# Performance work log

Measured on AMD Instinct MI355X. Metric: run time of the kernel, lower is better.

Reference implementation:

```python
import jax, jax.numpy as jnp
import numpy as np

L, N, T = 2048, 32, 200
V, IN, H, Q = 34, 512, 256, 256


def setup_inputs() -> dict:
    key = jax.random.key(0)
    ks = jax.random.split(key, 16)
    s = 0.05
    def rn(i, shape):
        return jax.random.normal(ks[i], shape, dtype=jnp.float32) * s
    zeros = lambda shape: jnp.zeros(shape, jnp.float32)
    return {
        "seqs": jax.random.normal(ks[0], (L, N, IN), dtype=jnp.float32),
        "seq_lens": L // 2 + jax.random.randint(ks[1], (N,), 0, L // 2),
        "label_in": jax.random.randint(ks[2], (N, T), 0, V),
        "embedding": rn(3, (V, H)),
        "inith": zeros((3, H)),
        "initc": zeros((3, H)),
        "W_ih0": rn(4, (4 * H, 2 * H)), "W_hh0": rn(5, (4 * H, H)),
        "b_ih0": zeros((4 * H,)), "b_hh0": zeros((4 * H,)),
        "W_ih1": rn(6, (4 * H, H)), "W_hh1": rn(7, (4 * H, H)),
        "b_ih1": zeros((4 * H,)), "b_hh1": zeros((4 * H,)),
        "W_ih2": rn(8, (4 * H, H)), "W_hh2": rn(9, (4 * H, H)),
        "b_ih2": zeros((4 * H,)), "b_hh2": zeros((4 * H,)),
        "Wq": rn(10, (Q, H)), "bq": zeros((Q,)),
        "Wk": rn(11, (Q, IN)), "bk": zeros((Q,)),
        "Wv": rn(12, (H, IN)), "bv": zeros((H,)),
        "Wo1": rn(13, (H, H + Q)), "bo1": zeros((H,)),
        "bo2": zeros((V,)),
    }


def _lstm_cell(x, h, c, Wih, Whh, bih, bhh):
    # torch.nn.LSTMCell gate math (i, f, g, o ordering)
    g = x @ Wih.T + bih + h @ Whh.T + bhh
    i, f, gg, o = jnp.split(g, 4, axis=-1)
    c_new = jax.nn.sigmoid(f) * c + jax.nn.sigmoid(i) * jnp.tanh(gg)
    h_new = jax.nn.sigmoid(o) * jnp.tanh(c_new)
    return h_new, c_new


def reference(seqs, seq_lens, label_in, embedding, inith, initc,
              W_ih0, W_hh0, b_ih0, b_hh0, W_ih1, W_hh1, b_ih1, b_hh1,
              W_ih2, W_hh2, b_ih2, b_hh2, Wq, bq, Wk, bk, Wv, bv, Wo1, bo1, bo2):
    Lk, Nk = seqs.shape[0], seqs.shape[1]
    Hh = inith.shape[1]

    # key/value projections: (L,N,IN) -> (N,L,Q) / (N,L,H)
    key_t = jnp.einsum('lni,qi->nlq', seqs, Wk) + bk
    val_t = jnp.einsum('lni,hi->nlh', seqs, Wv) + bv
    mask = (jnp.arange(Lk)[None, :] < seq_lens[:, None]).astype(seqs.dtype)  # (N,L)

    def attend(q):
        scores = jnp.einsum('nlq,nq->nl', key_t, q)
        attn = jax.nn.softmax(scores, axis=1)
        # faithful to torch: mask AFTER softmax, clamp, renormalize
        attn = jnp.maximum(attn * mask, 1e-9)
        attn = attn / attn.sum(axis=1, keepdims=True)
        return jnp.einsum('nl,nlh->nh', attn, val_t)

    h0 = jnp.broadcast_to(inith[0], (Nk, Hh)); c0 = jnp.broadcast_to(initc[0], (Nk, Hh))
    h1 = jnp.broadcast_to(inith[1], (Nk, Hh)); c1 = jnp.broadcast_to(initc[1], (Nk, Hh))
    h2 = jnp.broadcast_to(inith[2], (Nk, Hh)); c2 = jnp.broadcast_to(initc[2], (Nk, Hh))

    ctx = attend(h2 @ Wq.T + bq)
    emb = jnp.swapaxes(embedding[label_in], 0, 1)  # (T,N,H)

    def step(carry, x):
        h0, c0, h1, c1, h2, c2, ctx = carry
        rnn_in = jnp.concatenate([ctx, x], axis=1)  # (N, 2H)
        h0, c0 = _lstm_cell(rnn_in, h0, c0, W_ih0, W_hh0, b_ih0, b_hh0)
        h1, c1 = _lstm_cell(h0, h1, c1, W_ih1, W_hh1, b_ih1, b_hh1)
        h2, c2 = _lstm_cell(h1, h2, c2, W_ih2, W_hh2, b_ih2, b_hh2)
        q = h2 @ Wq.T + bq
        ctx = attend(q)
        hid = jnp.concatenate([ctx, q], axis=1) @ Wo1.T + bo1
        logit = hid @ embedding.T + bo2  # tied output weight
        return (h0, c0, h1, c1, h2, c2, ctx), logit

    _, logits = jax.lax.scan(step, (h0, c0, h1, c1, h2, c2, ctx), emb)
    return logits  # (T, N, V)
```

## Files before the change

kernel.cpp:

```cpp
#include <hip/hip_runtime.h>
#include <stdint.h>


typedef __attribute__((ext_vector_type(8))) short short8;
typedef __attribute__((ext_vector_type(4))) short short4v;
typedef __attribute__((ext_vector_type(4))) float float4v;

__device__ __forceinline__ float b2f(unsigned short u) {
  union { unsigned u; float f; } x; x.u = ((unsigned)u) << 16; return x.f;
}
__device__ __forceinline__ unsigned short f2b(float f) {
  union { float f; unsigned u; } x; x.f = f;
  unsigned r = (x.u + 0x7fffu + ((x.u >> 16) & 1u)) >> 16;
  return (unsigned short)r;
}
__device__ __forceinline__ float sigm(float x) { return 1.f / (1.f + __expf(-x)); }
__device__ __forceinline__ float tanh_s(float x) { return 1.f - 2.f / (__expf(2.f * x) + 1.f); }

static constexpr size_t OFF_K2   = 0;
static constexpr size_t OFF_VAL  = OFF_K2  + 33554432;
static constexpr size_t OFF_WK2  = OFF_VAL + 33554432;
static constexpr size_t OFF_BK2  = OFF_WK2 + 262144;
static constexpr size_t OFF_WKB  = OFF_BK2 + 1024;
static constexpr size_t OFF_BQBK = OFF_WKB + 2048;
static constexpr size_t OFF_KB   = OFF_BQBK + 256;
static constexpr size_t OFF_CTXA = OFF_KB  + 262144;
static constexpr size_t OFF_CTXS = OFF_CTXA + 6586368;
static constexpr size_t OFF_H2A  = OFF_CTXS + 25856;
static constexpr size_t OFF_HST  = OFF_H2A + 3276800;
static constexpr size_t OFF_CST  = OFF_HST + 98304;
static constexpr size_t OFF_FLAG = OFF_CST + 98304;
static constexpr size_t OFF_C    = OFF_FLAG + 256;
static constexpr size_t cEMB   = OFF_C;
static constexpr size_t cINITH = cEMB   + 17408;
static constexpr size_t cINITC = cINITH + 1536;
static constexpr size_t cWIH0  = cINITC + 1536;
static constexpr size_t cWHH0  = cWIH0  + 1048576;
static constexpr size_t cBIH0  = cWHH0  + 524288;
static constexpr size_t cBHH0  = cBIH0  + 2048;
static constexpr size_t cWIH1  = cBHH0  + 2048;
static constexpr size_t cWHH1  = cWIH1  + 524288;
static constexpr size_t cBIH1  = cWHH1  + 524288;
static constexpr size_t cBHH1  = cBIH1  + 2048;
static constexpr size_t cWIH2  = cBHH1  + 2048;
static constexpr size_t cWHH2  = cWIH2  + 524288;
static constexpr size_t cBIH2  = cWHH2  + 524288;
static constexpr size_t cBHH2  = cBIH2  + 2048;
static constexpr size_t cWQ    = cBHH2  + 2048;
static constexpr size_t cBQ    = cWQ    + 131072;
static constexpr size_t cWK    = cBQ    + 512;
static constexpr size_t cBK    = cWK    + 262144;
static constexpr size_t cWV    = cBK    + 512;
static constexpr size_t cBV    = cWV    + 262144;
static constexpr size_t cWO1   = cBV    + 512;
static constexpr size_t cBO1   = cWO1   + 262144;
static constexpr size_t cBO2   = cBO1   + 512;
static constexpr size_t WS_REQ = cBO2 + 128;

__global__ void k_sentinel(unsigned short* out, int n) {
  int i = blockIdx.x * 256 + threadIdx.x;
  if (i < n) out[i] = f2b(12345.0f);
}

__global__ void k_detect(const unsigned* __restrict__ seqw, int* flag) {
  int lane = threadIdx.x;
  unsigned w = seqw[lane];
  float lo = b2f((unsigned short)(w & 0xFFFFu));
  float a = fabsf(lo);
  bool ok = (a > 1e-3f) && (a < 4.0f);
  unsigned long long m = __ballot(ok);
  if (lane == 0) *flag = (__popcll((unsigned long long)m) >= 32) ? 1 : 0;
}

struct ConvList {
  const void* src[24];
  unsigned long long dstoff[24];
  int n[24];
};
__global__ void k_conv(ConvList cl, char* ws, const int* __restrict__ flag) {
  const int ti = blockIdx.y;
  const int i = blockIdx.x * 256 + threadIdx.x;
  const int n = cl.n[ti];
  if (i >= n) return;
  unsigned short* dst = (unsigned short*)(ws + cl.dstoff[ti]);
  if (*flag) dst[i] = ((const unsigned short*)cl.src[ti])[i];
  else       dst[i] = f2b(((const float*)cl.src[ti])[i]);
}

__global__ void k_p0(const unsigned short* __restrict__ Wq, const unsigned short* __restrict__ Wk,
                     const unsigned short* __restrict__ bq, const unsigned short* __restrict__ bk,
                     unsigned short* Wk2, float* bk2, float* wkb, float* bqbk) {
  int wg = blockIdx.x, tid = threadIdx.x;
  if (wg < 512) {
    int idx = wg * 256 + tid;
    int h = idx >> 9, j = idx & 511;
    float acc = 0.f;
    for (int i = 0; i < 256; ++i) acc += b2f(Wq[i * 256 + h]) * b2f(Wk[i * 512 + j]);
    Wk2[h * 512 + j] = f2b(acc);
  } else if (wg == 512) {
    float acc = 0.f;
    for (int i = 0; i < 256; ++i) acc += b2f(bk[i]) * b2f(Wq[i * 256 + tid]);
    bk2[tid] = acc;
  } else if (wg == 513) {
    for (int j = tid; j < 512; j += 256) {
      float acc = 0.f;
      for (int i = 0; i < 256; ++i) acc += b2f(bq[i]) * b2f(Wk[i * 512 + j]);
      wkb[j] = acc;
    }
  } else {
    if (tid == 0) {
      float acc = 0.f;
      for (int i = 0; i < 256; ++i) acc += b2f(bq[i]) * b2f(bk[i]);
      *bqbk = acc;
    }
  }
}

__global__ void k_init(const void* __restrict__ seqsv, const int* __restrict__ flag,
                       const unsigned short* __restrict__ inith, const unsigned short* __restrict__ initc,
                       const float* __restrict__ wkb, const float* __restrict__ bqbk, float* KB,
                       float* ctxacc, float* ctxsum, unsigned short* hst, float* cst) {
  int gid = blockIdx.x * 256 + threadIdx.x;
  for (int i = gid; i < 201 * 8192; i += 131072) ctxacc[i] = 0.f;
  if (gid < 6432) ctxsum[gid] = 0.f;
  if (gid < 8192) {
    int j = gid & 255;
    for (int Lr = 0; Lr < 3; ++Lr) {
      unsigned short hv = inith[Lr * 256 + j];
      hst[Lr * 16384 + gid] = hv;
      hst[Lr * 16384 + 8192 + gid] = hv;
      cst[Lr * 8192 + gid] = b2f(initc[Lr * 256 + j]);
    }
  }
  if (gid < 65536) {
    int l = gid >> 5, n = gid & 31;
    float acc = *bqbk;
    if (*flag) {
      const short8* row = (const short8*)((const unsigned short*)seqsv + (size_t)gid * 512);
      for (int jj = 0; jj < 64; ++jj) {
        short8 s = row[jj];
        #pragma unroll
        for (int e = 0; e < 8; ++e) acc += b2f((unsigned short)s[e]) * wkb[jj * 8 + e];
      }
    } else {
      const float4v* row = (const float4v*)((const float*)seqsv + (size_t)gid * 512);
      for (int jj = 0; jj < 128; ++jj) {
        float4v s = row[jj];
        acc += s.x * wkb[jj * 4 + 0] + s.y * wkb[jj * 4 + 1]
             + s.z * wkb[jj * 4 + 2] + s.w * wkb[jj * 4 + 3];
      }
    }
    KB[n * 2048 + l] = acc;
  }
}

__global__ __launch_bounds__(256) void k_gemm(
    const void* __restrict__ Aseqv, const int* __restrict__ flag,
    const unsigned short* __restrict__ Wk2,
    const unsigned short* __restrict__ Wv, const float* __restrict__ bk2,
    const unsigned short* __restrict__ bv, unsigned short* __restrict__ K2,
    unsigned short* __restrict__ VALo) {
  __shared__ short As[5120];
  __shared__ short Bs[5120];
  const int tid = threadIdx.x;
  const int lane = tid & 63, wid = tid >> 6;
  const int c0 = blockIdx.x * 128;
  const int m0 = blockIdx.y * 128;
  const unsigned short* Wb = (c0 < 256) ? Wk2 : Wv;
  const int cb = c0 & 255;
  const int srow = tid >> 1, skh = (tid & 1) * 16;
  const int m = lane & 15, q = lane >> 4;
  const bool isf32 = (*flag == 0);

  float4v zero = {0.f, 0.f, 0.f, 0.f};
  float4v acc[2][8];
  for (int i = 0; i < 2; ++i) for (int j = 0; j < 8; ++j) acc[i][j] = zero;

  for (int it = 0; it < 16; ++it) {
    const int k0 = it * 32;
    if (isf32) {
      const float4v* sa = (const float4v*)((const float*)Aseqv + (size_t)(m0 + srow) * 512 + k0 + skh);
      float4v u0 = sa[0], u1 = sa[1], u2 = sa[2], u3 = sa[3];
      short8 s0, s1;
      s0[0]=(short)f2b(u0.x); s0[1]=(short)f2b(u0.y); s0[2]=(short)f2b(u0.z); s0[3]=(short)f2b(u0.w);
      s0[4]=(short)f2b(u1.x); s0[5]=(short)f2b(u1.y); s0[6]=(short)f2b(u1.z); s0[7]=(short)f2b(u1.w);
      s1[0]=(short)f2b(u2.x); s1[1]=(short)f2b(u2.y); s1[2]=(short)f2b(u2.z); s1[3]=(short)f2b(u2.w);
      s1[4]=(short)f2b(u3.x); s1[5]=(short)f2b(u3.y); s1[6]=(short)f2b(u3.z); s1[7]=(short)f2b(u3.w);
      *(short8*)&As[srow * 40 + skh] = s0;
      *(short8*)&As[srow * 40 + skh + 8] = s1;
    } else {
      const short8* sa = (const short8*)((const unsigned short*)Aseqv + (size_t)(m0 + srow) * 512 + k0 + skh);
      *(short8*)&As[srow * 40 + skh] = sa[0];
      *(short8*)&As[srow * 40 + skh + 8] = sa[1];
    }
    const short8* sb = (const short8*)(Wb + (size_t)(cb + srow) * 512 + k0 + skh);
    *(short8*)&Bs[srow * 40 + skh] = sb[0];
    *(short8*)&Bs[srow * 40 + skh + 8] = sb[1];
    __syncthreads();
    short8 af[2], bf[8];
    #pragma unroll
    for (int i = 0; i < 2; ++i) af[i] = *(const short8*)&As[((wid * 2 + i) * 16 + m) * 40 + q * 8];
    #pragma unroll
    for (int j = 0; j < 8; ++j) bf[j] = *(const short8*)&Bs[(j * 16 + m) * 40 + q * 8];
    #pragma unroll
    for (int i = 0; i < 2; ++i)
      #pragma unroll
      for (int j = 0; j < 8; ++j)
        acc[i][j] = __builtin_amdgcn_mfma_f32_16x16x32_bf16(af[i], bf[j], acc[i][j], 0, 0, 0);
    __syncthreads();
  }
  const bool isK = (c0 < 256);
  #pragma unroll
  for (int i = 0; i < 2; ++i) {
    #pragma unroll
    for (int j = 0; j < 8; ++j) {
      const int colg = c0 + j * 16 + m;
      const float badd = isK ? bk2[colg] : b2f(bv[colg - 256]);
      #pragma unroll
      for (int r = 0; r < 4; ++r) {
        const int mm = m0 + (wid * 2 + i) * 16 + q * 4 + r;
        const int l = mm >> 5, n = mm & 31;
        const float v = acc[i][j][r] + badd;
        const size_t o = ((size_t)n * 2048 + l) * 256 + (isK ? colg : colg - 256);
        (isK ? K2 : VALo)[o] = f2b(v);
      }
    }
  }
}

__global__ __launch_bounds__(256) void k_attn(
    const int* __restrict__ seq_lens, const unsigned short* __restrict__ K2,
    const unsigned short* __restrict__ VAL, const float* __restrict__ KB,
    const unsigned short* __restrict__ h2src, float* __restrict__ ctxa_slot,
    float* __restrict__ ctxs_slot) {
  __shared__ float red[4][260];
  const int tid = threadIdx.x, wg = blockIdx.x;
  const int lane = tid & 63, wid = tid >> 6;
  const int n = wg >> 3, ch = wg & 7;
  const int len = seq_lens[n];
  const int l0 = ch << 8;
  int l1 = l0 + 256; if (l1 > len) l1 = len;
  const int hb = lane * 4;
  const float h0v = b2f(h2src[n * 256 + hb + 0]);
  const float h1v = b2f(h2src[n * 256 + hb + 1]);
  const float h2v = b2f(h2src[n * 256 + hb + 2]);
  const float h3v = b2f(h2src[n * 256 + hb + 3]);
  float a0 = 0.f, a1 = 0.f, a2 = 0.f, a3 = 0.f, se = 0.f;
  const float* kbn = KB + n * 2048;
  #pragma unroll 2
  for (int l = l0 + wid; l < l1; l += 4) {
    const size_t base = ((size_t)n * 2048 + l) * 256 + hb;
    const short4v kv = *(const short4v*)(K2 + base);
    float s = b2f((unsigned short)kv[0]) * h0v + b2f((unsigned short)kv[1]) * h1v
            + b2f((unsigned short)kv[2]) * h2v + b2f((unsigned short)kv[3]) * h3v;
    s += __shfl_xor(s, 1);  s += __shfl_xor(s, 2);  s += __shfl_xor(s, 4);
    s += __shfl_xor(s, 8);  s += __shfl_xor(s, 16); s += __shfl_xor(s, 32);
    float sc = s + kbn[l];
    sc = fminf(fmaxf(sc, -60.f), 60.f);
    const float e = __expf(sc);
    se += e;
    const short4v vv = *(const short4v*)(VAL + base);
    a0 += e * b2f((unsigned short)vv[0]); a1 += e * b2f((unsigned short)vv[1]);
    a2 += e * b2f((unsigned short)vv[2]); a3 += e * b2f((unsigned short)vv[3]);
  }
  red[wid][hb + 0] = a0; red[wid][hb + 1] = a1;
  red[wid][hb + 2] = a2; red[wid][hb + 3] = a3;
  if (lane == 0) red[wid][256] = se;
  __syncthreads();
  const float s = red[0][tid] + red[1][tid] + red[2][tid] + red[3][tid];
  atomicAdd(ctxa_slot + n * 256 + tid, s);
  if (tid == 0) {
    const float ssum = red[0][256] + red[1][256] + red[2][256] + red[3][256];
    atomicAdd(ctxs_slot + n, ssum);
  }
}

__global__ __launch_bounds__(256) void k_cell0(
    const float* __restrict__ ctxa_t, const float* __restrict__ ctxs_t,
    const int* __restrict__ label_in, int t, const unsigned short* __restrict__ emb,
    const unsigned short* __restrict__ Wih0, const unsigned short* __restrict__ Whh0,
    const unsigned short* __restrict__ bih0, const unsigned short* __restrict__ bhh0,
    const unsigned short* __restrict__ h0r, unsigned short* __restrict__ h0w,
    float* __restrict__ cst0) {
  __shared__ unsigned short lds_ctx[32 * 264];
  const int tid = threadIdx.x, wg = blockIdx.x;
  const int lane = tid & 63, wid = tid >> 6;
  for (int idx = tid; idx < 8192; idx += 256) {
    const int n = idx >> 8, k = idx & 255;
    lds_ctx[n * 264 + k] = f2b(ctxa_t[idx] / fmaxf(ctxs_t[n], 1e-30f));
  }
  __syncthreads();
  const int w = wg * 4 + wid;
  const int c = lane & 15, q = lane >> 4;
  const int grow = (c >> 2) * 256 + 4 * w + (c & 3);
  float4v ar0 = {0.f, 0.f, 0.f, 0.f}, ar1 = ar0;
  #pragma unroll
  for (int kk = 0; kk < 8; ++kk) {
    const int k = kk * 32 + q * 8;
    const short8 b = *(const short8*)(Wih0 + (size_t)grow * 512 + k);
    const short8 a0 = *(const short8*)&lds_ctx[c * 264 + k];
    const short8 a1 = *(const short8*)&lds_ctx[(c + 16) * 264 + k];
    ar0 = __builtin_amdgcn_mfma_f32_16x16x32_bf16(a0, b, ar0, 0, 0, 0);
    ar1 = __builtin_amdgcn_mfma_f32_16x16x32_bf16(a1, b, ar1, 0, 0, 0);
  }
  const int v0i = label_in[c * 200 + t];
  const int v1i = label_in[(c + 16) * 200 + t];
  const unsigned short* e0 = emb + (size_t)v0i * 256;
  const unsigned short* e1 = emb + (size_t)v1i * 256;
  #pragma unroll
  for (int kk = 0; kk < 8; ++kk) {
    const int k = kk * 32 + q * 8;
    const short8 b = *(const short8*)(Wih0 + (size_t)grow * 512 + 256 + k);
    const short8 a0 = *(const short8*)(e0 + k);
    const short8 a1 = *(const short8*)(e1 + k);
    ar0 = __builtin_amdgcn_mfma_f32_16x16x32_bf16(a0, b, ar0, 0, 0, 0);
    ar1 = __builtin_amdgcn_mfma_f32_16x16x32_bf16(a1, b, ar1, 0, 0, 0);
  }
  #pragma unroll
  for (int kk = 0; kk < 8; ++kk) {
    const int k = kk * 32 + q * 8;
    const short8 b = *(const short8*)(Whh0 + (size_t)grow * 256 + k);
    const short8 a0 = *(const short8*)(h0r + (size_t)c * 256 + k);
    const short8 a1 = *(const short8*)(h0r + (size_t)(c + 16) * 256 + k);
    ar0 = __builtin_amdgcn_mfma_f32_16x16x32_bf16(a0, b, ar0, 0, 0, 0);
    ar1 = __builtin_amdgcn_mfma_f32_16x16x32_bf16(a1, b, ar1, 0, 0, 0);
  }
  const float bias = b2f(bih0[grow]) + b2f(bhh0[grow]);
  const int d = c & 3, gt = c >> 2;
  #pragma unroll
  for (int mt = 0; mt < 2; ++mt) {
    const float4v av = mt ? ar1 : ar0;
    #pragma unroll
    for (int r = 0; r < 4; ++r) {
      const float g = av[r] + bias;
      const float gi = __shfl(g, (lane & 48) | d);
      const float gf = __shfl(g, (lane & 48) | (4 + d));
      const float gg = __shfl(g, (lane & 48) | (8 + d));
      const float go = __shfl(g, (lane & 48) | (12 + d));
      if (gt == 0) {
        const int n = mt * 16 + q * 4 + r;
        const int j = 4 * w + d;
        const float cold = cst0[n * 256 + j];
        const float cnew = sigm(gf) * cold + sigm(gi) * tanh_s(gg);
        const float hnew = sigm(go) * tanh_s(cnew);
        cst0[n * 256 + j] = cnew;
        h0w[n * 256 + j] = f2b(hnew);
      }
    }
  }
}

__global__ __launch_bounds__(256) void k_cell12(
    const unsigned short* __restrict__ Wih, const unsigned short* __restrict__ Whh,
    const unsigned short* __restrict__ bih, const unsigned short* __restrict__ bhh,
    const unsigned short* __restrict__ xsrc, const unsigned short* __restrict__ hsrc,
    float* __restrict__ cstate, unsigned short* __restrict__ hdst,
    unsigned short* __restrict__ h2dst) {
  const int tid = threadIdx.x, wg = blockIdx.x;
  const int lane = tid & 63, wid = tid >> 6;
  const int w = wg * 4 + wid;
  const int c = lane & 15, q = lane >> 4;
  const int grow = (c >> 2) * 256 + 4 * w + (c & 3);
  float4v ar0 = {0.f, 0.f, 0.f, 0.f}, ar1 = ar0;
  #pragma unroll
  for (int kk = 0; kk < 8; ++kk) {
    const int k = kk * 32 + q * 8;
    const short8 b = *(const short8*)(Wih + (size_t)grow * 256 + k);
    const short8 a0 = *(const short8*)(xsrc + (size_t)c * 256 + k);
    const short8 a1 = *(const short8*)(xsrc + (size_t)(c + 16) * 256 + k);
    ar0 = __builtin_amdgcn_mfma_f32_16x16x32_bf16(a0, b, ar0, 0, 0, 0);
    ar1 = __builtin_amdgcn_mfma_f32_16x16x32_bf16(a1, b, ar1, 0, 0, 0);
  }
  #pragma unroll
  for (int kk = 0; kk < 8; ++kk) {
    const int k = kk * 32 + q * 8;
    const short8 b = *(const short8*)(Whh + (size_t)grow * 256 + k);
    const short8 a0 = *(const short8*)(hsrc + (size_t)c * 256 + k);
    const short8 a1 = *(const short8*)(hsrc + (size_t)(c + 16) * 256 + k);
    ar0 = __builtin_amdgcn_mfma_f32_16x16x32_bf16(a0, b, ar0, 0, 0, 0);
    ar1 = __builtin_amdgcn_mfma_f32_16x16x32_bf16(a1, b, ar1, 0, 0, 0);
  }
  const float bias = b2f(bih[grow]) + b2f(bhh[grow]);
  const int d = c & 3, gt = c >> 2;
  #pragma unroll
  for (int mt = 0; mt < 2; ++mt) {
    const float4v av = mt ? ar1 : ar0;
    #pragma unroll
    for (int r = 0; r < 4; ++r) {
      const float g = av[r] + bias;
      const float gi = __shfl(g, (lane & 48) | d);
      const float gf = __shfl(g, (lane & 48) | (4 + d));
      const float gg = __shfl(g, (lane & 48) | (8 + d));
      const float go = __shfl(g, (lane & 48) | (12 + d));
      if (gt == 0) {
        const int n = mt * 16 + q * 4 + r;
        const int j = 4 * w + d;
        const float cold = cstate[n * 256 + j];
        const float cnew = sigm(gf) * cold + sigm(gi) * tanh_s(gg);
        const float hnew = sigm(go) * tanh_s(cnew);
        cstate[n * 256 + j] = cnew;
        hdst[n * 256 + j] = f2b(hnew);
        if (h2dst) h2dst[n * 256 + j] = f2b(hnew);
      }
    }
  }
}

__global__ __launch_bounds__(256) void k_out(
    const unsigned short* __restrict__ h2all, const float* __restrict__ ctxacc,
    const float* __restrict__ ctxsum,
    const unsigned short* __restrict__ Wq, const unsigned short* __restrict__ bq,
    const unsigned short* __restrict__ Wo1, const unsigned short* __restrict__ bo1,
    const unsigned short* __restrict__ emb, const unsigned short* __restrict__ bo2,
    void* __restrict__ outv, const int* __restrict__ flag) {
  const int wg = blockIdx.x, tid = threadIdx.x;
  const int g0 = wg * 4;
  __shared__ float z[4][512];
  __shared__ float hid[4][256];
  #pragma unroll
  for (int r = 0; r < 4; ++r) hid[r][tid] = b2f(h2all[(size_t)(g0 + r) * 256 + tid]);
  __syncthreads();
  {
    float qa[4] = {0.f, 0.f, 0.f, 0.f};
    const short8* wrow = (const short8*)(Wq + (size_t)tid * 256);
    for (int k8 = 0; k8 < 32; ++k8) {
      const short8 w = wrow[k8];
      float wf[8];
      #pragma unroll
      for (int e = 0; e < 8; ++e) wf[e] = b2f((unsigned short)w[e]);
      #pragma unroll
      for (int r = 0; r < 4; ++r) {
        const float* hz = &hid[r][k8 * 8];
        const float4v x0 = *(const float4v*)hz;
        const float4v x1 = *(const float4v*)(hz + 4);
        qa[r] += wf[0] * x0.x + wf[1] * x0.y + wf[2] * x0.z + wf[3] * x0.w
               + wf[4] * x1.x + wf[5] * x1.y + wf[6] * x1.z + wf[7] * x1.w;
      }
    }
    const float bqv = b2f(bq[tid]);
    #pragma unroll
    for (int r = 0; r < 4; ++r) z[r][256 + tid] = qa[r] + bqv;
    #pragma unroll
    for (int r = 0; r < 4; ++r) {
      const int row = g0 + r; const int tt = row >> 5; const int n = row & 31;
      const float ds = fmaxf(ctxsum[(tt + 1) * 32 + n], 1e-30f);
      z[r][tid] = ctxacc[(size_t)(tt + 1) * 8192 + n * 256 + tid] / ds;
    }
  }
  __syncthreads();
  {
    float ha[4] = {0.f, 0.f, 0.f, 0.f};
    const short8* wrow = (const short8*)(Wo1 + (size_t)tid * 512);
    for (int k8 = 0; k8 < 64; ++k8) {
      const short8 w = wrow[k8];
      float wf[8];
      #pragma unroll
      for (int e = 0; e < 8; ++e) wf[e] = b2f((unsigned short)w[e]);
      #pragma unroll
      for (int r = 0; r < 4; ++r) {
        const float* hz = &z[r][k8 * 8];
        const float4v x0 = *(const float4v*)hz;
        const float4v x1 = *(const float4v*)(hz + 4);
        ha[r] += wf[0] * x0.x + wf[1] * x0.y + wf[2] * x0.z + wf[3] * x0.w
               + wf[4] * x1.x + wf[5] * x1.y + wf[6] * x1.z + wf[7] * x1.w;
      }
    }
    const float bo = b2f(bo1[tid]);
    __syncthreads();
    #pragma unroll
    for (int r = 0; r < 4; ++r) hid[r][tid] = ha[r] + bo;
  }
  __syncthreads();
  if (tid < 136) {
    const int r = tid / 34, v = tid - r * 34;
    const unsigned short* er = emb + v * 256;
    float acc = b2f(bo2[v]);
    for (int h8 = 0; h8 < 32; ++h8) {
      const short8 ee = *(const short8*)(er + h8 * 8);
      const float* hz = &hid[r][h8 * 8];
      acc += b2f((unsigned short)ee[0]) * hz[0] + b2f((unsigned short)ee[1]) * hz[1]
           + b2f((unsigned short)ee[2]) * hz[2] + b2f((unsigned short)ee[3]) * hz[3]
           + b2f((unsigned short)ee[4]) * hz[4] + b2f((unsigned short)ee[5]) * hz[5]
           + b2f((unsigned short)ee[6]) * hz[6] + b2f((unsigned short)ee[7]) * hz[7];
    }
    const size_t oidx = (size_t)(g0 + r) * 34 + v;
    if (*flag) ((unsigned short*)outv)[oidx] = f2b(acc);
    else       ((float*)outv)[oidx] = acc;
  }
}

extern "C" void kernel_launch(void* const* d_in, const int* in_sizes, int n_in,
                              void* d_out, int out_size, void* d_ws, size_t ws_size,
                              hipStream_t stream) {
  const void* seqs    = d_in[0];
  const int* seq_lens = (const int*)d_in[1];
  const int* label_in = (const int*)d_in[2];

  if (ws_size < WS_REQ) {
    k_sentinel<<<dim3((out_size + 255) / 256), dim3(256), 0, stream>>>((unsigned short*)d_out, out_size);
    return;
  }

  char* ws = (char*)d_ws;
  unsigned short* K2   = (unsigned short*)(ws + OFF_K2);
  unsigned short* VALp = (unsigned short*)(ws + OFF_VAL);
  unsigned short* Wk2  = (unsigned short*)(ws + OFF_WK2);
  float* bk2  = (float*)(ws + OFF_BK2);
  float* wkb  = (float*)(ws + OFF_WKB);
  float* bqbk = (float*)(ws + OFF_BQBK);
  float* KB   = (float*)(ws + OFF_KB);
  float* ctxa = (float*)(ws + OFF_CTXA);
  float* ctxs = (float*)(ws + OFF_CTXS);
  unsigned short* h2all = (unsigned short*)(ws + OFF_H2A);
  unsigned short* hst   = (unsigned short*)(ws + OFF_HST);
  float* cst  = (float*)(ws + OFF_CST);
  int* flag   = (int*)(ws + OFF_FLAG);

  k_detect<<<dim3(1), dim3(64), 0, stream>>>((const unsigned*)seqs, flag);

  static const size_t dsto[24] = {
    cEMB, cINITH, cINITC, cWIH0, cWHH0, cBIH0, cBHH0, cWIH1, cWHH1, cBIH1, cBHH1,
    cWIH2, cWHH2, cBIH2, cBHH2, cWQ, cBQ, cWK, cBK, cWV, cBV, cWO1, cBO1, cBO2 };
  ConvList cl;
  for (int i = 0; i < 24; ++i) {
    cl.src[i] = d_in[3 + i];
    cl.dstoff[i] = dsto[i];
    cl.n[i] = in_sizes[3 + i];
  }
  k_conv<<<dim3(2048, 24), dim3(256), 0, stream>>>(cl, ws, flag);

  const unsigned short* emb   = (const unsigned short*)(ws + cEMB);
  const unsigned short* inith = (const unsigned short*)(ws + cINITH);
  const unsigned short* initc = (const unsigned short*)(ws + cINITC);
  const unsigned short* Wih0  = (const unsigned short*)(ws + cWIH0);
  const unsigned short* Whh0  = (const unsigned short*)(ws + cWHH0);
  const unsigned short* bih0  = (const unsigned short*)(ws + cBIH0);
  const unsigned short* bhh0  = (const unsigned short*)(ws + cBHH0);
  const unsigned short* Wih1  = (const unsigned short*)(ws + cWIH1);
  const unsigned short* Whh1  = (const unsigned short*)(ws + cWHH1);
  const unsigned short* bih1  = (const unsigned short*)(ws + cBIH1);
  const unsigned short* bhh1  = (const unsigned short*)(ws + cBHH1);
  const unsigned short* Wih2  = (const unsigned short*)(ws + cWIH2);
  const unsigned short* Whh2  = (const unsigned short*)(ws + cWHH2);
  const unsigned short* bih2  = (const unsigned short*)(ws + cBIH2);
  const unsigned short* bhh2  = (const unsigned short*)(ws + cBHH2);
  const unsigned short* Wq    = (const unsigned short*)(ws + cWQ);
  const unsigned short* bq    = (const unsigned short*)(ws + cBQ);
  const unsigned short* Wk    = (const unsigned short*)(ws + cWK);
  const unsigned short* bk    = (const unsigned short*)(ws + cBK);
  const unsigned short* Wv    = (const unsigned short*)(ws + cWV);
  const unsigned short* bv    = (const unsigned short*)(ws + cBV);
  const unsigned short* Wo1   = (const unsigned short*)(ws + cWO1);
  const unsigned short* bo1   = (const unsigned short*)(ws + cBO1);
  const unsigned short* bo2   = (const unsigned short*)(ws + cBO2);

  k_p0<<<dim3(515), dim3(256), 0, stream>>>(Wq, Wk, bq, bk, Wk2, bk2, wkb, bqbk);
  k_init<<<dim3(512), dim3(256), 0, stream>>>(seqs, flag, inith, initc, wkb, bqbk, KB, ctxa, ctxs, hst, cst);
  k_gemm<<<dim3(4, 512), dim3(256), 0, stream>>>(seqs, flag, Wk2, Wv, bk2, bv, K2, VALp);

  k_attn<<<dim3(256), dim3(256), 0, stream>>>(seq_lens, K2, VALp, KB, hst + 32768, ctxa, ctxs);

  for (int t = 0; t < 200; ++t) {
    const int p = t & 1, pn = 1 - p;
    unsigned short* h0r = hst + p * 8192;
    unsigned short* h0w = hst + pn * 8192;
    unsigned short* h1r = hst + 16384 + p * 8192;
    unsigned short* h1w = hst + 16384 + pn * 8192;
    unsigned short* h2r = hst + 32768 + p * 8192;
    unsigned short* h2w = hst + 32768 + pn * 8192;

    k_cell0<<<dim3(16), dim3(256), 0, stream>>>(ctxa + (size_t)t * 8192, ctxs + (size_t)t * 32,
                                                label_in, t, emb, Wih0, Whh0, bih0, bhh0,
                                                h0r, h0w, cst);
    k_cell12<<<dim3(16), dim3(256), 0, stream>>>(Wih1, Whh1, bih1, bhh1, h0w, h1r,
                                                 cst + 8192, h1w, (unsigned short*)nullptr);
    k_cell12<<<dim3(16), dim3(256), 0, stream>>>(Wih2, Whh2, bih2, bhh2, h1w, h2r,
                                                 cst + 16384, h2w, h2all + (size_t)t * 8192);
    k_attn<<<dim3(256), dim3(256), 0, stream>>>(seq_lens, K2, VALp, KB, h2w,
                                                ctxa + (size_t)(t + 1) * 8192,
                                                ctxs + (size_t)(t + 1) * 32);
  }

  k_out<<<dim3(1600), dim3(256), 0, stream>>>(h2all, ctxa, ctxs, Wq, bq, Wo1, bo1, emb, bo2, d_out, flag);
}
```

Baseline: 14.63 ms.

## Fuse decoder time loop into one persistent cooperative kernel with grid syncs

Replaces the 800 per-timestep kernel launches (cell0, two cell12, attention) with a single cooperative persistent kernel that loops over the 200 steps and uses grid-wide barriers between stages. The goal is to remove launch and inter-kernel gap overhead on a latency-bound recurrence. In exchange, each step now pays four grid.sync barriers, and most blocks sit idle during the LSTM cell stages. Attention work is strided over up to 256 blocks sized by the CU count.

```diff
diff --git a/kernel.cpp b/kernel.cpp
--- a/kernel.cpp
+++ b/kernel.cpp
@@ -1,5 +1,8 @@
 #include <hip/hip_runtime.h>
+#include <hip/hip_cooperative_groups.h>
 #include <stdint.h>
+
+namespace cg = cooperative_groups;
 
 
 typedef __attribute__((ext_vector_type(8))) short short8;
@@ -228,181 +231,215 @@
   }
 }
 
-__global__ __launch_bounds__(256) void k_attn(
-    const int* __restrict__ seq_lens, const unsigned short* __restrict__ K2,
-    const unsigned short* __restrict__ VAL, const float* __restrict__ KB,
-    const unsigned short* __restrict__ h2src, float* __restrict__ ctxa_slot,
-    float* __restrict__ ctxs_slot) {
-  __shared__ float red[4][260];
-  const int tid = threadIdx.x, wg = blockIdx.x;
-  const int lane = tid & 63, wid = tid >> 6;
-  const int n = wg >> 3, ch = wg & 7;
-  const int len = seq_lens[n];
-  const int l0 = ch << 8;
-  int l1 = l0 + 256; if (l1 > len) l1 = len;
-  const int hb = lane * 4;
-  const float h0v = b2f(h2src[n * 256 + hb + 0]);
-  const float h1v = b2f(h2src[n * 256 + hb + 1]);
-  const float h2v = b2f(h2src[n * 256 + hb + 2]);
-  const float h3v = b2f(h2src[n * 256 + hb + 3]);
-  float a0 = 0.f, a1 = 0.f, a2 = 0.f, a3 = 0.f, se = 0.f;
-  const float* kbn = KB + n * 2048;
-  #pragma unroll 2
-  for (int l = l0 + wid; l < l1; l += 4) {
-    const size_t base = ((size_t)n * 2048 + l) * 256 + hb;
-    const short4v kv = *(const short4v*)(K2 + base);
-    float s = b2f((unsigned short)kv[0]) * h0v + b2f((unsigned short)kv[1]) * h1v
-            + b2f((unsigned short)kv[2]) * h2v + b2f((unsigned short)kv[3]) * h3v;
-    s += __shfl_xor(s, 1);  s += __shfl_xor(s, 2);  s += __shfl_xor(s, 4);
-    s += __shfl_xor(s, 8);  s += __shfl_xor(s, 16); s += __shfl_xor(s, 32);
-    float sc = s + kbn[l];
-    sc = fminf(fmaxf(sc, -60.f), 60.f);
-    const float e = __expf(sc);
-    se += e;
-    const short4v vv = *(const short4v*)(VAL + base);
-    a0 += e * b2f((unsigned short)vv[0]); a1 += e * b2f((unsigned short)vv[1]);
-    a2 += e * b2f((unsigned short)vv[2]); a3 += e * b2f((unsigned short)vv[3]);
-  }
-  red[wid][hb + 0] = a0; red[wid][hb + 1] = a1;
-  red[wid][hb + 2] = a2; red[wid][hb + 3] = a3;
-  if (lane == 0) red[wid][256] = se;
-  __syncthreads();
-  const float s = red[0][tid] + red[1][tid] + red[2][tid] + red[3][tid];
-  atomicAdd(ctxa_slot + n * 256 + tid, s);
-  if (tid == 0) {
-    const float ssum = red[0][256] + red[1][256] + red[2][256] + red[3][256];
-    atomicAdd(ctxs_slot + n, ssum);
-  }
-}
-
-__global__ __launch_bounds__(256) void k_cell0(
-    const float* __restrict__ ctxa_t, const float* __restrict__ ctxs_t,
-    const int* __restrict__ label_in, int t, const unsigned short* __restrict__ emb,
+__global__ __launch_bounds__(256) void k_dec(
+    const int* __restrict__ seq_lens, const int* __restrict__ label_in,
+    const unsigned short* __restrict__ emb,
     const unsigned short* __restrict__ Wih0, const unsigned short* __restrict__ Whh0,
     const unsigned short* __restrict__ bih0, const unsigned short* __restrict__ bhh0,
-    const unsigned short* __restrict__ h0r, unsigned short* __restrict__ h0w,
-    float* __restrict__ cst0) {
+    const unsigned short* __restrict__ Wih1, const unsigned short* __restrict__ Whh1,
+    const unsigned short* __restrict__ bih1, const unsigned short* __restrict__ bhh1,
+    const unsigned short* __restrict__ Wih2, const unsigned short* __restrict__ Whh2,
+    const unsigned short* __restrict__ bih2, const unsigned short* __restrict__ bhh2,
+    const unsigned short* __restrict__ K2, const unsigned short* __restrict__ VALi,
+    const float* __restrict__ KB,
+    float* ctxacc, float* ctxsum, unsigned short* hst, float* cstates,
+    unsigned short* h2all) {
+  const int wg = blockIdx.x, G = gridDim.x;
+  const int tid = threadIdx.x;
+  const int lane = tid & 63, wid = tid >> 6;
+  cg::grid_group grid = cg::this_grid();
+  __shared__ float red[4][260];
   __shared__ unsigned short lds_ctx[32 * 264];
-  const int tid = threadIdx.x, wg = blockIdx.x;
-  const int lane = tid & 63, wid = tid >> 6;
-  for (int idx = tid; idx < 8192; idx += 256) {
-    const int n = idx >> 8, k = idx & 255;
-    lds_ctx[n * 264 + k] = f2b(ctxa_t[idx] / fmaxf(ctxs_t[n], 1e-30f));
-  }
-  __syncthreads();
-  const int w = wg * 4 + wid;
-  const int c = lane & 15, q = lane >> 4;
-  const int grow = (c >> 2) * 256 + 4 * w + (c & 3);
-  float4v ar0 = {0.f, 0.f, 0.f, 0.f}, ar1 = ar0;
-  #pragma unroll
-  for (int kk = 0; kk < 8; ++kk) {
-    const int k = kk * 32 + q * 8;
-    const short8 b = *(const short8*)(Wih0 + (size_t)grow * 512 + k);
-    const short8 a0 = *(const short8*)&lds_ctx[c * 264 + k];
-    const short8 a1 = *(const short8*)&lds_ctx[(c + 16) * 264 + k];
-    ar0 = __builtin_amdgcn_mfma_f32_16x16x32_bf16(a0, b, ar0, 0, 0, 0);
-    ar1 = __builtin_amdgcn_mfma_f32_16x16x32_bf16(a1, b, ar1, 0, 0, 0);
-  }
-  const int v0i = label_in[c * 200 + t];
-  const int v1i = label_in[(c + 16) * 200 + t];
-  const unsigned short* e0 = emb + (size_t)v0i * 256;
-  const unsigned short* e1 = emb + (size_t)v1i * 256;
-  #pragma unroll
-  for (int kk = 0; kk < 8; ++kk) {
-    const int k = kk * 32 + q * 8;
-    const short8 b = *(const short8*)(Wih0 + (size_t)grow * 512 + 256 + k);
-    const short8 a0 = *(const short8*)(e0 + k);
-    const short8 a1 = *(const short8*)(e1 + k);
-    ar0 = __builtin_amdgcn_mfma_f32_16x16x32_bf16(a0, b, ar0, 0, 0, 0);
-    ar1 = __builtin_amdgcn_mfma_f32_16x16x32_bf16(a1, b, ar1, 0, 0, 0);
-  }
-  #pragma unroll
-  for (int kk = 0; kk < 8; ++kk) {
-    const int k = kk * 32 + q * 8;
-    const short8 b = *(const short8*)(Whh0 + (size_t)grow * 256 + k);
-    const short8 a0 = *(const short8*)(h0r + (size_t)c * 256 + k);
-    const short8 a1 = *(const short8*)(h0r + (size_t)(c + 16) * 256 + k);
-    ar0 = __builtin_amdgcn_mfma_f32_16x16x32_bf16(a0, b, ar0, 0, 0, 0);
-    ar1 = __builtin_amdgcn_mfma_f32_16x16x32_bf16(a1, b, ar1, 0, 0, 0);
-  }
-  const float bias = b2f(bih0[grow]) + b2f(bhh0[grow]);
-  const int d = c & 3, gt = c >> 2;
-  #pragma unroll
-  for (int mt = 0; mt < 2; ++mt) {
-    const float4v av = mt ? ar1 : ar0;
-    #pragma unroll
-    for (int r = 0; r < 4; ++r) {
-      const float g = av[r] + bias;
-      const float gi = __shfl(g, (lane & 48) | d);
-      const float gf = __shfl(g, (lane & 48) | (4 + d));
-      const float gg = __shfl(g, (lane & 48) | (8 + d));
-      const float go = __shfl(g, (lane & 48) | (12 + d));
-      if (gt == 0) {
-        const int n = mt * 16 + q * 4 + r;
-        const int j = 4 * w + d;
-        const float cold = cst0[n * 256 + j];
-        const float cnew = sigm(gf) * cold + sigm(gi) * tanh_s(gg);
-        const float hnew = sigm(go) * tanh_s(cnew);
-        cst0[n * 256 + j] = cnew;
-        h0w[n * 256 + j] = f2b(hnew);
-      }
-    }
-  }
-}
-
-__global__ __launch_bounds__(256) void k_cell12(
-    const unsigned short* __restrict__ Wih, const unsigned short* __restrict__ Whh,
-    const unsigned short* __restrict__ bih, const unsigned short* __restrict__ bhh,
-    const unsigned short* __restrict__ xsrc, const unsigned short* __restrict__ hsrc,
-    float* __restrict__ cstate, unsigned short* __restrict__ hdst,
-    unsigned short* __restrict__ h2dst) {
-  const int tid = threadIdx.x, wg = blockIdx.x;
-  const int lane = tid & 63, wid = tid >> 6;
-  const int w = wg * 4 + wid;
-  const int c = lane & 15, q = lane >> 4;
-  const int grow = (c >> 2) * 256 + 4 * w + (c & 3);
-  float4v ar0 = {0.f, 0.f, 0.f, 0.f}, ar1 = ar0;
-  #pragma unroll
-  for (int kk = 0; kk < 8; ++kk) {
-    const int k = kk * 32 + q * 8;
-    const short8 b = *(const short8*)(Wih + (size_t)grow * 256 + k);
-    const short8 a0 = *(const short8*)(xsrc + (size_t)c * 256 + k);
-    const short8 a1 = *(const short8*)(xsrc + (size_t)(c + 16) * 256 + k);
-    ar0 = __builtin_amdgcn_mfma_f32_16x16x32_bf16(a0, b, ar0, 0, 0, 0);
-    ar1 = __builtin_amdgcn_mfma_f32_16x16x32_bf16(a1, b, ar1, 0, 0, 0);
-  }
-  #pragma unroll
-  for (int kk = 0; kk < 8; ++kk) {
-    const int k = kk * 32 + q * 8;
-    const short8 b = *(const short8*)(Whh + (size_t)grow * 256 + k);
-    const short8 a0 = *(const short8*)(hsrc + (size_t)c * 256 + k);
-    const short8 a1 = *(const short8*)(hsrc + (size_t)(c + 16) * 256 + k);
-    ar0 = __builtin_amdgcn_mfma_f32_16x16x32_bf16(a0, b, ar0, 0, 0, 0);
-    ar1 = __builtin_amdgcn_mfma_f32_16x16x32_bf16(a1, b, ar1, 0, 0, 0);
-  }
-  const float bias = b2f(bih[grow]) + b2f(bhh[grow]);
-  const int d = c & 3, gt = c >> 2;
-  #pragma unroll
-  for (int mt = 0; mt < 2; ++mt) {
-    const float4v av = mt ? ar1 : ar0;
-    #pragma unroll
-    for (int r = 0; r < 4; ++r) {
-      const float g = av[r] + bias;
-      const float gi = __shfl(g, (lane & 48) | d);
-      const float gf = __shfl(g, (lane & 48) | (4 + d));
-      const float gg = __shfl(g, (lane & 48) | (8 + d));
-      const float go = __shfl(g, (lane & 48) | (12 + d));
-      if (gt == 0) {
-        const int n = mt * 16 + q * 4 + r;
-        const int j = 4 * w + d;
-        const float cold = cstate[n * 256 + j];
-        const float cnew = sigm(gf) * cold + sigm(gi) * tanh_s(gg);
-        const float hnew = sigm(go) * tanh_s(cnew);
-        cstate[n * 256 + j] = cnew;
-        hdst[n * 256 + j] = f2b(hnew);
-        if (h2dst) h2dst[n * 256 + j] = f2b(hnew);
-      }
-    }
+
+  auto attn = [&](int slot, const unsigned short* h2src) {
+    for (int base = 0; base < 256; base += G) {
+      const int pr = base + wg;
+      const bool act = (pr < 256);
+      const int n = act ? (pr >> 3) : 0;
+      const int ch = pr & 7;
+      const int len = seq_lens[n];
+      const int l0 = ch << 8;
+      int l1 = l0 + 256; if (l1 > len) l1 = len;
+      if (!act) l1 = l0;
+      const int hb = lane * 4;
+      const float h0v = b2f(h2src[n * 256 + hb + 0]);
+      const float h1v = b2f(h2src[n * 256 + hb + 1]);
+      const float h2v = b2f(h2src[n * 256 + hb + 2]);
+      const float h3v = b2f(h2src[n * 256 + hb + 3]);
+      float a0 = 0.f, a1 = 0.f, a2 = 0.f, a3 = 0.f, se = 0.f;
+      const float* kbn = KB + n * 2048;
+      #pragma unroll 2
+      for (int l = l0 + wid; l < l1; l += 4) {
+        const size_t base2 = ((size_t)n * 2048 + l) * 256 + hb;
+        const short4v kv = *(const short4v*)(K2 + base2);
+        float s = b2f((unsigned short)kv[0]) * h0v + b2f((unsigned short)kv[1]) * h1v
+                + b2f((unsigned short)kv[2]) * h2v + b2f((unsigned short)kv[3]) * h3v;
+        s += __shfl_xor(s, 1);  s += __shfl_xor(s, 2);  s += __shfl_xor(s, 4);
+        s += __shfl_xor(s, 8);  s += __shfl_xor(s, 16); s += __shfl_xor(s, 32);
+        float sc = s + kbn[l];
+        sc = fminf(fmaxf(sc, -60.f), 60.f);
+        const float e = __expf(sc);
+        se += e;
+        const short4v vv = *(const short4v*)(VALi + base2);
+        a0 += e * b2f((unsigned short)vv[0]); a1 += e * b2f((unsigned short)vv[1]);
+        a2 += e * b2f((unsigned short)vv[2]); a3 += e * b2f((unsigned short)vv[3]);
+      }
+      red[wid][hb + 0] = a0; red[wid][hb + 1] = a1;
+      red[wid][hb + 2] = a2; red[wid][hb + 3] = a3;
+      if (lane == 0) red[wid][256] = se;
+      __syncthreads();
+      if (act) {
+        const float s = red[0][tid] + red[1][tid] + red[2][tid] + red[3][tid];
+        atomicAdd(ctxacc + (size_t)slot * 8192 + n * 256 + tid, s);
+        if (tid == 0) {
+          const float ssum = red[0][256] + red[1][256] + red[2][256] + red[3][256];
+          atomicAdd(ctxsum + slot * 32 + n, ssum);
+        }
+      }
+      __syncthreads();
+    }
+  };
+
+  auto cell12 = [&](const unsigned short* Wih, const unsigned short* Whh,
+                    const unsigned short* bih, const unsigned short* bhh,
+                    const unsigned short* xsrc, const unsigned short* hsrc,
+                    float* cstate, unsigned short* hdst, unsigned short* h2dst) {
+    const int w = wg * 4 + wid;
+    const int c = lane & 15, q = lane >> 4;
+    const int grow = (c >> 2) * 256 + 4 * w + (c & 3);
+    float4v ar0 = {0.f, 0.f, 0.f, 0.f}, ar1 = ar0;
+    #pragma unroll
+    for (int kk = 0; kk < 8; ++kk) {
+      const int k = kk * 32 + q * 8;
+      const short8 b = *(const short8*)(Wih + (size_t)grow * 256 + k);
+      const short8 a0 = *(const short8*)(xsrc + (size_t)c * 256 + k);
+      const short8 a1 = *(const short8*)(xsrc + (size_t)(c + 16) * 256 + k);
+      ar0 = __builtin_amdgcn_mfma_f32_16x16x32_bf16(a0, b, ar0, 0, 0, 0);
+      ar1 = __builtin_amdgcn_mfma_f32_16x16x32_bf16(a1, b, ar1, 0, 0, 0);
+    }
+    #pragma unroll
+    for (int kk = 0; kk < 8; ++kk) {
+      const int k = kk * 32 + q * 8;
+      const short8 b = *(const short8*)(Whh + (size_t)grow * 256 + k);
+      const short8 a0 = *(const short8*)(hsrc + (size_t)c * 256 + k);
+      const short8 a1 = *(const short8*)(hsrc + (size_t)(c + 16) * 256 + k);
+      ar0 = __builtin_amdgcn_mfma_f32_16x16x32_bf16(a0, b, ar0, 0, 0, 0);
+      ar1 = __builtin_amdgcn_mfma_f32_16x16x32_bf16(a1, b, ar1, 0, 0, 0);
+    }
+    const float bias = b2f(bih[grow]) + b2f(bhh[grow]);
+    const int d = c & 3, gt = c >> 2;
+    #pragma unroll
+    for (int mt = 0; mt < 2; ++mt) {
+      const float4v av = mt ? ar1 : ar0;
+      #pragma unroll
+      for (int r = 0; r < 4; ++r) {
+        const float g = av[r] + bias;
+        const float gi = __shfl(g, (lane & 48) | d);
+        const float gf = __shfl(g, (lane & 48) | (4 + d));
+        const float gg = __shfl(g, (lane & 48) | (8 + d));
+        const float go = __shfl(g, (lane & 48) | (12 + d));
+        if (gt == 0) {
+          const int n = mt * 16 + q * 4 + r;
+          const int j = 4 * w + d;
+          const float cold = cstate[n * 256 + j];
+          const float cnew = sigm(gf) * cold + sigm(gi) * tanh_s(gg);
+          const float hnew = sigm(go) * tanh_s(cnew);
+          cstate[n * 256 + j] = cnew;
+          hdst[n * 256 + j] = f2b(hnew);
+          if (h2dst) h2dst[n * 256 + j] = f2b(hnew);
+        }
+      }
+    }
+  };
+
+  attn(0, hst + 32768);
+  grid.sync();
+
+  #pragma clang loop unroll(disable)
+  for (int t = 0; t < 200; ++t) {
+    const int p = t & 1;
+    unsigned short* h0r = hst + p * 8192;
+    unsigned short* h0w = hst + (1 - p) * 8192;
+    unsigned short* h1r = hst + 16384 + p * 8192;
+    unsigned short* h1w = hst + 16384 + (1 - p) * 8192;
+    unsigned short* h2r = hst + 32768 + p * 8192;
+    unsigned short* h2w = hst + 32768 + (1 - p) * 8192;
+
+    if (wg < 16) {
+      const float* ctxa_t = ctxacc + (size_t)t * 8192;
+      const float* ctxs_t = ctxsum + (size_t)t * 32;
+      for (int idx = tid; idx < 8192; idx += 256) {
+        const int n = idx >> 8, k = idx & 255;
+        lds_ctx[n * 264 + k] = f2b(ctxa_t[idx] / fmaxf(ctxs_t[n], 1e-30f));
+      }
+      __syncthreads();
+      const int w = wg * 4 + wid;
+      const int c = lane & 15, q = lane >> 4;
+      const int grow = (c >> 2) * 256 + 4 * w + (c & 3);
+      float4v ar0 = {0.f, 0.f, 0.f, 0.f}, ar1 = ar0;
+      #pragma unroll
+      for (int kk = 0; kk < 8; ++kk) {
+        const int k = kk * 32 + q * 8;
+        const short8 b = *(const short8*)(Wih0 + (size_t)grow * 512 + k);
+        const short8 a0 = *(const short8*)&lds_ctx[c * 264 + k];
+        const short8 a1 = *(const short8*)&lds_ctx[(c + 16) * 264 + k];
+        ar0 = __builtin_amdgcn_mfma_f32_16x16x32_bf16(a0, b, ar0, 0, 0, 0);
+        ar1 = __builtin_amdgcn_mfma_f32_16x16x32_bf16(a1, b, ar1, 0, 0, 0);
+      }
+      const int v0i = label_in[c * 200 + t];
+      const int v1i = label_in[(c + 16) * 200 + t];
+      const unsigned short* e0 = emb + (size_t)v0i * 256;
+      const unsigned short* e1 = emb + (size_t)v1i * 256;
+      #pragma unroll
+      for (int kk = 0; kk < 8; ++kk) {
+        const int k = kk * 32 + q * 8;
+        const short8 b = *(const short8*)(Wih0 + (size_t)grow * 512 + 256 + k);
+        const short8 a0 = *(const short8*)(e0 + k);
+        const short8 a1 = *(const short8*)(e1 + k);
+        ar0 = __builtin_amdgcn_mfma_f32_16x16x32_bf16(a0, b, ar0, 0, 0, 0);
+        ar1 = __builtin_amdgcn_mfma_f32_16x16x32_bf16(a1, b, ar1, 0, 0, 0);
+      }
+      #pragma unroll
+      for (int kk = 0; kk < 8; ++kk) {
+        const int k = kk * 32 + q * 8;
+        const short8 b = *(const short8*)(Whh0 + (size_t)grow * 256 + k);
+        const short8 a0 = *(const short8*)(h0r + (size_t)c * 256 + k);
+        const short8 a1 = *(const short8*)(h0r + (size_t)(c + 16) * 256 + k);
+        ar0 = __builtin_amdgcn_mfma_f32_16x16x32_bf16(a0, b, ar0, 0, 0, 0);
+        ar1 = __builtin_amdgcn_mfma_f32_16x16x32_bf16(a1, b, ar1, 0, 0, 0);
+      }
+      const float bias = b2f(bih0[grow]) + b2f(bhh0[grow]);
+      const int d = c & 3, gt = c >> 2;
+      #pragma unroll
+      for (int mt = 0; mt < 2; ++mt) {
+        const float4v av = mt ? ar1 : ar0;
+        #pragma unroll
+        for (int r = 0; r < 4; ++r) {
+          const float g = av[r] + bias;
+          const float gi = __shfl(g, (lane & 48) | d);
+          const float gf = __shfl(g, (lane & 48) | (4 + d));
+          const float gg = __shfl(g, (lane & 48) | (8 + d));
+          const float go = __shfl(g, (lane & 48) | (12 + d));
+          if (gt == 0) {
+            const int n = mt * 16 + q * 4 + r;
+            const int j = 4 * w + d;
+            const float cold = cstates[n * 256 + j];
+            const float cnew = sigm(gf) * cold + sigm(gi) * tanh_s(gg);
+            const float hnew = sigm(go) * tanh_s(cnew);
+            cstates[n * 256 + j] = cnew;
+            h0w[n * 256 + j] = f2b(hnew);
+          }
+        }
+      }
+      __syncthreads();
+    }
+    grid.sync();
+    if (wg < 16) cell12(Wih1, Whh1, bih1, bhh1, h0w, h1r, cstates + 8192, h1w, (unsigned short*)nullptr);
+    grid.sync();
+    if (wg < 16) cell12(Wih2, Whh2, bih2, bhh2, h1w, h2r, cstates + 16384, h2w, h2all + (size_t)t * 8192);
+    grid.sync();
+    attn(t + 1, h2w);
+    grid.sync();
   }
 }
 
@@ -558,28 +595,22 @@
   k_init<<<dim3(512), dim3(256), 0, stream>>>(seqs, flag, inith, initc, wkb, bqbk, KB, ctxa, ctxs, hst, cst);
   k_gemm<<<dim3(4, 512), dim3(256), 0, stream>>>(seqs, flag, Wk2, Wv, bk2, bv, K2, VALp);
 
-  k_attn<<<dim3(256), dim3(256), 0, stream>>>(seq_lens, K2, VALp, KB, hst + 32768, ctxa, ctxs);
-
-  for (int t = 0; t < 200; ++t) {
-    const int p = t & 1, pn = 1 - p;
-    unsigned short* h0r = hst + p * 8192;
-    unsigned short* h0w = hst + pn * 8192;
-    unsigned short* h1r = hst + 16384 + p * 8192;
-    unsigned short* h1w = hst + 16384 + pn * 8192;
-    unsigned short* h2r = hst + 32768 + p * 8192;
-    unsigned short* h2w = hst + 32768 + pn * 8192;
-
-    k_cell0<<<dim3(16), dim3(256), 0, stream>>>(ctxa + (size_t)t * 8192, ctxs + (size_t)t * 32,
-                                                label_in, t, emb, Wih0, Whh0, bih0, bhh0,
-                                                h0r, h0w, cst);
-    k_cell12<<<dim3(16), dim3(256), 0, stream>>>(Wih1, Whh1, bih1, bhh1, h0w, h1r,
-                                                 cst + 8192, h1w, (unsigned short*)nullptr);
-    k_cell12<<<dim3(16), dim3(256), 0, stream>>>(Wih2, Whh2, bih2, bhh2, h1w, h2r,
-                                                 cst + 16384, h2w, h2all + (size_t)t * 8192);
-    k_attn<<<dim3(256), dim3(256), 0, stream>>>(seq_lens, K2, VALp, KB, h2w,
-                                                ctxa + (size_t)(t + 1) * 8192,
-                                                ctxs + (size_t)(t + 1) * 32);
-  }
+  int dev = 0;
+  hipGetDevice(&dev);
+  int cus = 256;
+  hipDeviceGetAttribute(&cus, hipDeviceAttributeMultiprocessorCount, dev);
+  int G = cus < 256 ? cus : 256;
+  if (G < 16) G = 16;
+
+  void* kargs[] = {
+    (void*)&seq_lens, (void*)&label_in, (void*)&emb,
+    (void*)&Wih0, (void*)&Whh0, (void*)&bih0, (void*)&bhh0,
+    (void*)&Wih1, (void*)&Whh1, (void*)&bih1, (void*)&bhh1,
+    (void*)&Wih2, (void*)&Whh2, (void*)&bih2, (void*)&bhh2,
+    (void*)&K2, (void*)&VALp, (void*)&KB,
+    (void*)&ctxa, (void*)&ctxs, (void*)&hst, (void*)&cst, (void*)&h2all
+  };
+  hipLaunchCooperativeKernel((void*)k_dec, dim3(G), dim3(256), kargs, 0, stream);
 
   k_out<<<dim3(1600), dim3(256), 0, stream>>>(h2all, ctxa, ctxs, Wq, bq, Wo1, bo1, emb, bo2, d_out, flag);
 }
```

After: 33.08 ms. 2.26x slower.
